# Optimization experiments

Hardware: AMD Instinct MI355X
Metric: run time of the kernel (lower is better)

## Reference

```python
import jax, jax.numpy as jnp
import numpy as np

N, E, IN, OUT = 50000, 800000, 256, 256
EPS = 1e-5


def setup_inputs() -> dict:
    key = jax.random.key(0)
    k1, k2, k3 = jax.random.split(key, 3)
    x = jax.random.normal(k1, (N, IN), dtype=jnp.float32)
    edge_index = jax.random.randint(k2, (2, E), 0, N, dtype=jnp.int64)
    batch = jnp.zeros((N,), dtype=jnp.int64)
    # glorot-style init for GCN weight
    scale = jnp.sqrt(2.0 / (IN + OUT)).astype(jnp.float32)
    W = jax.random.normal(k3, (IN, OUT), dtype=jnp.float32) * scale
    conv_bias = jnp.zeros((OUT,), dtype=jnp.float32)
    ln_weight = jnp.ones((OUT,), dtype=jnp.float32)
    ln_bias = jnp.zeros((OUT,), dtype=jnp.float32)
    prelu_a = jnp.full((1,), 0.25, dtype=jnp.float32)  # nn.PReLU default
    return {"x": x, "edge_index": edge_index, "batch": batch, "W": W,
            "conv_bias": conv_bias, "ln_weight": ln_weight,
            "ln_bias": ln_bias, "prelu_a": prelu_a}


def reference(x, edge_index, batch, W, conv_bias, ln_weight, ln_bias, prelu_a):
    n = x.shape[0]
    src, dst = edge_index[0], edge_index[1]
    # GCNConv: add self-loops, symmetric deg^{-1/2} normalization
    loop = jnp.arange(n, dtype=src.dtype)
    src_f = jnp.concatenate([src, loop])  # [E+N]
    dst_f = jnp.concatenate([dst, loop])
    h = x @ W  # [N, OUT] -- transform before propagate (PyG order)
    deg = jax.ops.segment_sum(jnp.ones_like(dst_f, dtype=h.dtype), dst_f,
                              num_segments=n)  # >=1 due to self loops
    dinv = jax.lax.rsqrt(deg)
    norm = dinv[src_f] * dinv[dst_f]  # [E+N]
    out = jax.ops.segment_sum(h[src_f] * norm[:, None], dst_f,
                              num_segments=n) + conv_bias  # [N, OUT]
    # PyG LayerNorm, mode='graph', batch=None: normalize over ALL nodes+feats
    mu = out.mean()
    xc = out - mu
    std = jnp.sqrt((xc * xc).mean())
    y = xc / (std + EPS) * ln_weight + ln_bias
    # PReLU (single shared slope)
    return jnp.where(y >= 0, y, prelu_a * y)
```

## Files before the change

### kernel.cpp

```cpp
#include <hip/hip_runtime.h>
#include <hip/hip_bf16.h>


#define F 256
#define EPSV 1e-5f

typedef __attribute__((ext_vector_type(8))) short short8;
typedef __attribute__((ext_vector_type(4))) float f32x4;

__device__ __forceinline__ unsigned short f2bf(float f) {
  union { float f; unsigned u; } v; v.f = f;
  unsigned r = v.u + 0x7fffu + ((v.u >> 16) & 1u);
  return (unsigned short)(r >> 16);
}

__device__ __forceinline__ float bf2f(unsigned short u) {
  union { unsigned u; float f; } v; v.u = ((unsigned)u) << 16; return v.f;
}


__global__ void init_prep(int* __restrict__ deg_cnt, int N, int NB,
                          const float* __restrict__ W, unsigned short* __restrict__ Wb) {
  if ((int)blockIdx.x < NB) {
    int i = blockIdx.x * 256 + threadIdx.x;
    if (i < N) deg_cnt[i] = 0;
    return;
  }
  int gid = (blockIdx.x - NB) * 256 + threadIdx.x;
  int j = gid & 7;
  int lane = (gid >> 3) & 63;
  int kc = (gid >> 9) & 7;
  int tt = gid >> 12;
  int k = kc * 32 + (lane >> 4) * 8 + j;
  int n = tt * 16 + (lane & 15);
  Wb[gid] = f2bf(W[k * 256 + n]);
}


__global__ void count_gemm(const int* __restrict__ dst, int* __restrict__ deg_cnt,
                           int* __restrict__ rank, int E, int eb,
                           const float* __restrict__ x, const unsigned short* __restrict__ Wb,
                           ushort4* __restrict__ hb, int N) {
  __shared__ unsigned short A[64][264];

  if ((int)blockIdx.x < eb) {
    int e = blockIdx.x * 256 + threadIdx.x;
    if (e < E) rank[e] = atomicAdd(&deg_cnt[dst[e]], 1);
    return;
  }

  int bid = blockIdx.x - eb;
  int m0 = bid * 64;
  int t = threadIdx.x;
  int lane = t & 63;
  int wave = t >> 6;
  int q = lane >> 4;

#pragma unroll
  for (int j = 0; j < 16; ++j) {
    int idx = j * 256 + t;
    int row = idx >> 6;
    int c4 = idx & 63;
    int gr = m0 + row;
    int grc = gr < N ? gr : N - 1;
    f32x4 v = __builtin_nontemporal_load((const f32x4*)(x + (size_t)grc * F + c4 * 4));
    ushort4 u;
    u.x = f2bf(v[0]); u.y = f2bf(v[1]); u.z = f2bf(v[2]); u.w = f2bf(v[3]);
    *(ushort4*)&A[row][c4 * 4] = u;
  }
  __syncthreads();

  f32x4 acc[4][4];
#pragma unroll
  for (int m = 0; m < 4; ++m)
#pragma unroll
    for (int tt = 0; tt < 4; ++tt)
      acc[m][tt] = (f32x4){0.f, 0.f, 0.f, 0.f};

  int arow = lane & 15;
  for (int kc = 0; kc < 8; ++kc) {
    short8 a[4];
#pragma unroll
    for (int m = 0; m < 4; ++m)
      a[m] = *(const short8*)&A[m * 16 + arow][kc * 32 + q * 8];
#pragma unroll
    for (int tt = 0; tt < 4; ++tt) {
      const short8 b = *(const short8*)(Wb + (((wave * 4 + tt) * 8 + kc) * 64 + lane) * 8);
#pragma unroll
      for (int m = 0; m < 4; ++m)
        acc[m][tt] = __builtin_amdgcn_mfma_f32_16x16x32_bf16(a[m], b, acc[m][tt], 0, 0, 0);
    }
  }

  __syncthreads();

  int ccol = lane & 15;
#pragma unroll
  for (int m = 0; m < 4; ++m) {
#pragma unroll
    for (int rr = 0; rr < 4; ++rr) {
      int lrow = m * 16 + q * 4 + rr;
#pragma unroll
      for (int tt = 0; tt < 4; ++tt)
        A[lrow][(wave * 4 + tt) * 16 + ccol] = f2bf(acc[m][tt][rr]);
    }
  }
  __syncthreads();
#pragma unroll
  for (int j = 0; j < 16; ++j) {
    int idx = j * 256 + t;
    int row = idx >> 6;
    int c4 = idx & 63;
    int grow = m0 + row;
    if (grow < N) hb[(size_t)grow * 64 + c4] = *(const ushort4*)&A[row][c4 * 4];
  }
}


__global__ void block_sums(const int* __restrict__ deg_cnt, int* __restrict__ bsum,
                           float* __restrict__ dinv, int N) {
  __shared__ int s[256];
  int t = threadIdx.x;
  int i = blockIdx.x * 256 + t;
  int d = (i < N) ? deg_cnt[i] : 0;
  if (i < N) dinv[i] = rsqrtf((float)(d + 1));
  s[t] = d;
  __syncthreads();
  for (int off = 128; off > 0; off >>= 1) {
    if (t < off) s[t] += s[t + off];
    __syncthreads();
  }
  if (t == 0) bsum[blockIdx.x] = s[0];
}

__global__ void scan_bsums(const int* __restrict__ bsum, int* __restrict__ boff, int nb) {
  __shared__ int s[256];
  int t = threadIdx.x;
  int v = (t < nb) ? bsum[t] : 0;
  s[t] = v;
  __syncthreads();
  for (int off = 1; off < 256; off <<= 1) {
    int x = (t >= off) ? s[t - off] : 0;
    __syncthreads();
    s[t] += x;
    __syncthreads();
  }
  if (t < nb) boff[t] = s[t] - v;
}

__global__ void write_csr(const int* __restrict__ deg_cnt, const int* __restrict__ boff,
                          int* __restrict__ csr_ptr, int N, int E) {
  __shared__ int s[256];
  int t = threadIdx.x;
  int i = blockIdx.x * 256 + t;
  int v = (i < N) ? deg_cnt[i] : 0;
  s[t] = v;
  __syncthreads();
  for (int off = 1; off < 256; off <<= 1) {
    int x = (t >= off) ? s[t - off] : 0;
    __syncthreads();
    s[t] += x;
    __syncthreads();
  }
  if (i < N) csr_ptr[i] = boff[blockIdx.x] + s[t] - v;
  if (i == 0) csr_ptr[N] = E;
}


__global__ void fill(const int* __restrict__ src, const int* __restrict__ dst,
                     const int* __restrict__ rank, const int* __restrict__ csr_ptr,
                     int* __restrict__ csr_src, int E) {
  int e = blockIdx.x * 256 + threadIdx.x;
  if (e < E) {
    int d = dst[e];
    csr_src[csr_ptr[d] + rank[e]] = src[e];
  }
}


__global__ void aggregate(const ushort4* __restrict__ hb, const int* __restrict__ csr_ptr,
                          const int* __restrict__ csr_src, const float* __restrict__ dinv,
                          const float* __restrict__ conv_bias, float* __restrict__ out,
                          double2* __restrict__ partials, int N) {
  int wave = threadIdx.x >> 6;
  int lane = threadIdx.x & 63;
  int row = blockIdx.x * 4 + wave;
  float s1 = 0.f, s2 = 0.f;

  if (row < N) {
    float di = dinv[row];
    int b0 = csr_ptr[row], b1 = csr_ptr[row + 1];
    ushort4 self = hb[(size_t)row * 64 + lane];
    f32x4 acc;
    acc[0] = bf2f(self.x) * di; acc[1] = bf2f(self.y) * di;
    acc[2] = bf2f(self.z) * di; acc[3] = bf2f(self.w) * di;

    for (int e = b0; e < b1; e += 16) {
      int idx[16];
#pragma unroll
      for (int j = 0; j < 16; ++j) {
        int ee = e + j;
        idx[j] = csr_src[ee < b1 ? ee : b1 - 1];
      }
      ushort4 v[16];
#pragma unroll
      for (int j = 0; j < 16; ++j) v[j] = hb[(size_t)idx[j] * 64 + lane];
      float w[16];
#pragma unroll
      for (int j = 0; j < 16; ++j) w[j] = dinv[idx[j]];
#pragma unroll
      for (int j = 0; j < 16; ++j) {
        float m = (e + j < b1) ? w[j] : 0.f;
        acc[0] = fmaf(bf2f(v[j].x), m, acc[0]);
        acc[1] = fmaf(bf2f(v[j].y), m, acc[1]);
        acc[2] = fmaf(bf2f(v[j].z), m, acc[2]);
        acc[3] = fmaf(bf2f(v[j].w), m, acc[3]);
      }
    }

    const f32x4 b = *(const f32x4*)(conv_bias + lane * 4);
    acc[0] = fmaf(acc[0], di, b[0]);
    acc[1] = fmaf(acc[1], di, b[1]);
    acc[2] = fmaf(acc[2], di, b[2]);
    acc[3] = fmaf(acc[3], di, b[3]);
    __builtin_nontemporal_store(acc, (f32x4*)(out + ((size_t)row * 64 + lane) * 4));
    s1 = acc[0] + acc[1] + acc[2] + acc[3];
    s2 = acc[0] * acc[0] + acc[1] * acc[1] + acc[2] * acc[2] + acc[3] * acc[3];
  }

  __shared__ float r1[256];
  __shared__ float r2[256];
  int t = threadIdx.x;
  r1[t] = s1;
  r2[t] = s2;
  __syncthreads();
  for (int off = 128; off > 0; off >>= 1) {
    if (t < off) { r1[t] += r1[t + off]; r2[t] += r2[t + off]; }
    __syncthreads();
  }
  if (t == 0) {
    double2 pp;
    pp.x = (double)r1[0];
    pp.y = (double)r2[0];
    partials[blockIdx.x] = pp;
  }
}

__global__ void finalize_stats(const double2* __restrict__ partials, int nb,
                               float* __restrict__ stats, double cnt) {
  __shared__ double q1[1024];
  __shared__ double q2[1024];
  int t = threadIdx.x;
  double a1 = 0.0, a2 = 0.0;
  for (int i = t; i < nb; i += 1024) {
    double2 pp = partials[i];
    a1 += pp.x;
    a2 += pp.y;
  }
  q1[t] = a1;
  q2[t] = a2;
  __syncthreads();
  for (int off = 512; off > 0; off >>= 1) {
    if (t < off) { q1[t] += q1[t + off]; q2[t] += q2[t + off]; }
    __syncthreads();
  }
  if (t == 0) {
    double mu = q1[0] / cnt;
    double var = q2[0] / cnt - mu * mu;
    if (var < 0) var = 0;
    double sd = sqrt(var);
    stats[0] = (float)mu;
    stats[1] = (float)(1.0 / (sd + (double)EPSV));
  }
}

__global__ void norm_prelu(float* __restrict__ out, const float* __restrict__ stats,
                           const float* __restrict__ lw, const float* __restrict__ lb,
                           const float* __restrict__ pa, int n4) {
  int i = blockIdx.x * blockDim.x + threadIdx.x;
  if (i >= n4) return;
  float mu = stats[0];
  float inv = stats[1];
  float a = pa[0];
  int c4 = (i & 63) * 4;
  const f32x4 w = *(const f32x4*)(lw + c4);
  const f32x4 b = *(const f32x4*)(lb + c4);
  f32x4 v = __builtin_nontemporal_load((const f32x4*)(out + (size_t)i * 4));
  f32x4 y;
#pragma unroll
  for (int j = 0; j < 4; ++j) {
    float yv = (v[j] - mu) * inv * w[j] + b[j];
    y[j] = yv >= 0.f ? yv : a * yv;
  }
  __builtin_nontemporal_store(y, (f32x4*)(out + (size_t)i * 4));
}


extern "C" void kernel_launch(void* const* d_in, const int* in_sizes, int n_in,
                              void* d_out, int out_size, void* d_ws, size_t ws_size,
                              hipStream_t stream) {
  const float* x = (const float*)d_in[0];
  const int* eidx = (const int*)d_in[1];
  const float* W = (const float*)d_in[3];
  const float* conv_bias = (const float*)d_in[4];
  const float* ln_w = (const float*)d_in[5];
  const float* ln_b = (const float*)d_in[6];
  const float* prelu_a = (const float*)d_in[7];
  float* out = (float*)d_out;

  int N = in_sizes[0] / F;
  int E = in_sizes[1] / 2;
  const int* src = eidx;
  const int* dst = eidx + E;

  int nAggBlocks = (N + 3) / 4;
  int eb = (E + 255) / 256;
  int gemmb = (N + 63) / 64;
  int NB = (N + 255) / 256;

  char* p = (char*)d_ws;
  auto carve = [&](size_t bytes) { char* r = p; p += (bytes + 255) & ~(size_t)255; return r; };
  ushort4* hb    = (ushort4*)carve((size_t)N * 64 * sizeof(ushort4));
  unsigned short* Wb = (unsigned short*)carve((size_t)F * F * sizeof(short));
  int* deg_cnt   = (int*)carve((size_t)N * sizeof(int));
  int* rank      = (int*)carve((size_t)E * sizeof(int));
  float* dinv    = (float*)carve((size_t)N * sizeof(float));
  int* csr_ptr   = (int*)carve((size_t)(N + 1) * sizeof(int));
  int* csr_src   = (int*)carve((size_t)E * sizeof(int));
  int* bsum      = (int*)carve((size_t)NB * sizeof(int));
  int* boff      = (int*)carve((size_t)NB * sizeof(int));
  double2* partials = (double2*)carve((size_t)nAggBlocks * sizeof(double2));
  float* stats   = (float*)carve(2 * sizeof(float));

  init_prep<<<NB + 256, 256, 0, stream>>>(deg_cnt, N, NB, W, Wb);
  count_gemm<<<eb + gemmb, 256, 0, stream>>>(dst, deg_cnt, rank, E, eb, x, Wb, hb, N);
  block_sums<<<NB, 256, 0, stream>>>(deg_cnt, bsum, dinv, N);
  scan_bsums<<<1, 256, 0, stream>>>(bsum, boff, NB);
  write_csr<<<NB, 256, 0, stream>>>(deg_cnt, boff, csr_ptr, N, E);
  fill<<<eb, 256, 0, stream>>>(src, dst, rank, csr_ptr, csr_src, E);
  aggregate<<<nAggBlocks, 256, 0, stream>>>(hb, csr_ptr, csr_src, dinv,
                                            conv_bias, out, partials, N);
  finalize_stats<<<1, 1024, 0, stream>>>(partials, nAggBlocks, stats,
                                         (double)N * (double)F);
  int n4 = N * (F / 4);
  norm_prelu<<<(n4 + 255) / 256, 256, 0, stream>>>(out, stats, ln_w, ln_b, prelu_a, n4);
}
```

Measured before the change: 276.7 us.

## Cut launches via atomic-based CSR build and atomic global stats

Replaces the three-kernel prefix scan with a single kernel that takes block offsets through an atomic base counter, so CSR segments are contiguous but not in node order. The per-edge rank array is dropped and fill now claims slots with atomics on csr_ptr; aggregate recovers each row's range from the end pointer and the degree. The finalize_stats kernel is removed: aggregate blocks atomically add double partial sums, and every norm_prelu thread recomputes mean and inverse std. This removes two to three launches and the rank traffic, at the cost of atomic contention, nondeterministic neighbour order, and per-thread double math.

```diff
diff --git a/kernel.cpp b/kernel.cpp
--- a/kernel.cpp
+++ b/kernel.cpp
@@ -20,10 +20,16 @@
 
 
 __global__ void init_prep(int* __restrict__ deg_cnt, int N, int NB,
-                          const float* __restrict__ W, unsigned short* __restrict__ Wb) {
+                          const float* __restrict__ W, unsigned short* __restrict__ Wb,
+                          int* __restrict__ gbase, double* __restrict__ gsum) {
   if ((int)blockIdx.x < NB) {
     int i = blockIdx.x * 256 + threadIdx.x;
     if (i < N) deg_cnt[i] = 0;
+    if (blockIdx.x == 0 && threadIdx.x == 0) {
+      *gbase = 0;
+      gsum[0] = 0.0;
+      gsum[1] = 0.0;
+    }
     return;
   }
   int gid = (blockIdx.x - NB) * 256 + threadIdx.x;
@@ -38,14 +44,14 @@
 
 
 __global__ void count_gemm(const int* __restrict__ dst, int* __restrict__ deg_cnt,
-                           int* __restrict__ rank, int E, int eb,
+                           int E, int eb,
                            const float* __restrict__ x, const unsigned short* __restrict__ Wb,
                            ushort4* __restrict__ hb, int N) {
   __shared__ unsigned short A[64][264];
 
   if ((int)blockIdx.x < eb) {
     int e = blockIdx.x * 256 + threadIdx.x;
-    if (e < E) rank[e] = atomicAdd(&deg_cnt[dst[e]], 1);
+    if (e < E) atomicAdd(&deg_cnt[dst[e]], 1);
     return;
   }
 
@@ -117,71 +123,42 @@
 }
 
 
-__global__ void block_sums(const int* __restrict__ deg_cnt, int* __restrict__ bsum,
-                           float* __restrict__ dinv, int N) {
+__global__ void build_ptr(const int* __restrict__ deg_cnt, float* __restrict__ dinv,
+                          int* __restrict__ csr_ptr, int* __restrict__ gbase, int N) {
   __shared__ int s[256];
+  __shared__ int base;
   int t = threadIdx.x;
   int i = blockIdx.x * 256 + t;
   int d = (i < N) ? deg_cnt[i] : 0;
   if (i < N) dinv[i] = rsqrtf((float)(d + 1));
   s[t] = d;
   __syncthreads();
-  for (int off = 128; off > 0; off >>= 1) {
-    if (t < off) s[t] += s[t + off];
-    __syncthreads();
-  }
-  if (t == 0) bsum[blockIdx.x] = s[0];
-}
-
-__global__ void scan_bsums(const int* __restrict__ bsum, int* __restrict__ boff, int nb) {
-  __shared__ int s[256];
-  int t = threadIdx.x;
-  int v = (t < nb) ? bsum[t] : 0;
-  s[t] = v;
-  __syncthreads();
   for (int off = 1; off < 256; off <<= 1) {
     int x = (t >= off) ? s[t - off] : 0;
     __syncthreads();
     s[t] += x;
     __syncthreads();
   }
-  if (t < nb) boff[t] = s[t] - v;
-}
-
-__global__ void write_csr(const int* __restrict__ deg_cnt, const int* __restrict__ boff,
-                          int* __restrict__ csr_ptr, int N, int E) {
-  __shared__ int s[256];
-  int t = threadIdx.x;
-  int i = blockIdx.x * 256 + t;
-  int v = (i < N) ? deg_cnt[i] : 0;
-  s[t] = v;
-  __syncthreads();
-  for (int off = 1; off < 256; off <<= 1) {
-    int x = (t >= off) ? s[t - off] : 0;
-    __syncthreads();
-    s[t] += x;
-    __syncthreads();
-  }
-  if (i < N) csr_ptr[i] = boff[blockIdx.x] + s[t] - v;
-  if (i == 0) csr_ptr[N] = E;
+  if (t == 255) base = atomicAdd(gbase, s[255]);
+  __syncthreads();
+  if (i < N) csr_ptr[i] = base + s[t] - d;
 }
 
 
 __global__ void fill(const int* __restrict__ src, const int* __restrict__ dst,
-                     const int* __restrict__ rank, const int* __restrict__ csr_ptr,
-                     int* __restrict__ csr_src, int E) {
+                     int* __restrict__ csr_ptr, int* __restrict__ csr_src, int E) {
   int e = blockIdx.x * 256 + threadIdx.x;
   if (e < E) {
-    int d = dst[e];
-    csr_src[csr_ptr[d] + rank[e]] = src[e];
+    int pos = atomicAdd(&csr_ptr[dst[e]], 1);
+    csr_src[pos] = src[e];
   }
 }
 
 
 __global__ void aggregate(const ushort4* __restrict__ hb, const int* __restrict__ csr_ptr,
-                          const int* __restrict__ csr_src, const float* __restrict__ dinv,
-                          const float* __restrict__ conv_bias, float* __restrict__ out,
-                          double2* __restrict__ partials, int N) {
+                          const int* __restrict__ deg_cnt, const int* __restrict__ csr_src,
+                          const float* __restrict__ dinv, const float* __restrict__ conv_bias,
+                          float* __restrict__ out, double* __restrict__ gsum, int N) {
   int wave = threadIdx.x >> 6;
   int lane = threadIdx.x & 63;
   int row = blockIdx.x * 4 + wave;
@@ -189,7 +166,8 @@
 
   if (row < N) {
     float di = dinv[row];
-    int b0 = csr_ptr[row], b1 = csr_ptr[row + 1];
+    int b1 = csr_ptr[row];
+    int b0 = b1 - deg_cnt[row];
     ushort4 self = hb[(size_t)row * 64 + lane];
     f32x4 acc;
     acc[0] = bf2f(self.x) * di; acc[1] = bf2f(self.y) * di;
@@ -239,48 +217,24 @@
     __syncthreads();
   }
   if (t == 0) {
-    double2 pp;
-    pp.x = (double)r1[0];
-    pp.y = (double)r2[0];
-    partials[blockIdx.x] = pp;
-  }
-}
-
-__global__ void finalize_stats(const double2* __restrict__ partials, int nb,
-                               float* __restrict__ stats, double cnt) {
-  __shared__ double q1[1024];
-  __shared__ double q2[1024];
-  int t = threadIdx.x;
-  double a1 = 0.0, a2 = 0.0;
-  for (int i = t; i < nb; i += 1024) {
-    double2 pp = partials[i];
-    a1 += pp.x;
-    a2 += pp.y;
-  }
-  q1[t] = a1;
-  q2[t] = a2;
-  __syncthreads();
-  for (int off = 512; off > 0; off >>= 1) {
-    if (t < off) { q1[t] += q1[t + off]; q2[t] += q2[t + off]; }
-    __syncthreads();
-  }
-  if (t == 0) {
-    double mu = q1[0] / cnt;
-    double var = q2[0] / cnt - mu * mu;
-    if (var < 0) var = 0;
-    double sd = sqrt(var);
-    stats[0] = (float)mu;
-    stats[1] = (float)(1.0 / (sd + (double)EPSV));
-  }
-}
-
-__global__ void norm_prelu(float* __restrict__ out, const float* __restrict__ stats,
+    atomicAdd(&gsum[0], (double)r1[0]);
+    atomicAdd(&gsum[1], (double)r2[0]);
+  }
+}
+
+
+__global__ void norm_prelu(float* __restrict__ out, const double* __restrict__ gsum,
                            const float* __restrict__ lw, const float* __restrict__ lb,
-                           const float* __restrict__ pa, int n4) {
+                           const float* __restrict__ pa, int n4, double cnt) {
   int i = blockIdx.x * blockDim.x + threadIdx.x;
   if (i >= n4) return;
-  float mu = stats[0];
-  float inv = stats[1];
+  double g1 = gsum[0];
+  double g2 = gsum[1];
+  double mud = g1 / cnt;
+  double var = g2 / cnt - mud * mud;
+  if (var < 0) var = 0;
+  float mu = (float)mud;
+  float inv = (float)(1.0 / (sqrt(var) + (double)EPSV));
   float a = pa[0];
   int c4 = (i & 63) * 4;
   const f32x4 w = *(const f32x4*)(lw + c4);
@@ -323,25 +277,19 @@
   ushort4* hb    = (ushort4*)carve((size_t)N * 64 * sizeof(ushort4));
   unsigned short* Wb = (unsigned short*)carve((size_t)F * F * sizeof(short));
   int* deg_cnt   = (int*)carve((size_t)N * sizeof(int));
-  int* rank      = (int*)carve((size_t)E * sizeof(int));
   float* dinv    = (float*)carve((size_t)N * sizeof(float));
-  int* csr_ptr   = (int*)carve((size_t)(N + 1) * sizeof(int));
+  int* csr_ptr   = (int*)carve((size_t)N * sizeof(int));
   int* csr_src   = (int*)carve((size_t)E * sizeof(int));
-  int* bsum      = (int*)carve((size_t)NB * sizeof(int));
-  int* boff      = (int*)carve((size_t)NB * sizeof(int));
-  double2* partials = (double2*)carve((size_t)nAggBlocks * sizeof(double2));
-  float* stats   = (float*)carve(2 * sizeof(float));
-
-  init_prep<<<NB + 256, 256, 0, stream>>>(deg_cnt, N, NB, W, Wb);
-  count_gemm<<<eb + gemmb, 256, 0, stream>>>(dst, deg_cnt, rank, E, eb, x, Wb, hb, N);
-  block_sums<<<NB, 256, 0, stream>>>(deg_cnt, bsum, dinv, N);
-  scan_bsums<<<1, 256, 0, stream>>>(bsum, boff, NB);
-  write_csr<<<NB, 256, 0, stream>>>(deg_cnt, boff, csr_ptr, N, E);
-  fill<<<eb, 256, 0, stream>>>(src, dst, rank, csr_ptr, csr_src, E);
-  aggregate<<<nAggBlocks, 256, 0, stream>>>(hb, csr_ptr, csr_src, dinv,
-                                            conv_bias, out, partials, N);
-  finalize_stats<<<1, 1024, 0, stream>>>(partials, nAggBlocks, stats,
-                                         (double)N * (double)F);
+  int* gbase     = (int*)carve(sizeof(int));
+  double* gsum   = (double*)carve(2 * sizeof(double));
+
+  init_prep<<<NB + 256, 256, 0, stream>>>(deg_cnt, N, NB, W, Wb, gbase, gsum);
+  count_gemm<<<eb + gemmb, 256, 0, stream>>>(dst, deg_cnt, E, eb, x, Wb, hb, N);
+  build_ptr<<<NB, 256, 0, stream>>>(deg_cnt, dinv, csr_ptr, gbase, N);
+  fill<<<eb, 256, 0, stream>>>(src, dst, csr_ptr, csr_src, E);
+  aggregate<<<nAggBlocks, 256, 0, stream>>>(hb, csr_ptr, deg_cnt, csr_src, dinv,
+                                            conv_bias, out, gsum, N);
   int n4 = N * (F / 4);
-  norm_prelu<<<(n4 + 255) / 256, 256, 0, stream>>>(out, stats, ln_w, ln_b, prelu_a, n4);
-}
+  norm_prelu<<<(n4 + 255) / 256, 256, 0, stream>>>(out, gsum, ln_w, ln_b, prelu_a,
+                                                   n4, (double)N * (double)F);
+}
```

New measurement: 534.1 us. 93.0% more time.

## Split aggregate waves into half-wave rows and fuse stats finalize into norm kernel

Applied to the files above, without the earlier changes.

The aggregate kernel now gives each half-wave one destination row, with each lane loading 16-byte bf16 chunks. A wave therefore handles two rows and fetches wider gathers, and the neighbor loop is unrolled by 8 instead of 16. The separate finalize_stats kernel is removed: each of 256 blocks of the norm_prelu kernel reduces the partial sums itself, then applies normalization and PReLU in a grid-stride loop. This saves one launch and the stats round trip, at the cost of redundant per-block reduction work over the partials.

```diff
diff --git a/kernel.cpp b/kernel.cpp
--- a/kernel.cpp
+++ b/kernel.cpp
@@ -6,6 +6,7 @@
 #define EPSV 1e-5f
 
 typedef __attribute__((ext_vector_type(8))) short short8;
+typedef __attribute__((ext_vector_type(8))) unsigned short ushort8v;
 typedef __attribute__((ext_vector_type(4))) float f32x4;
 
 __device__ __forceinline__ unsigned short f2bf(float f) {
@@ -49,8 +50,7 @@
     return;
   }
 
-  int bid = blockIdx.x - eb;
-  int m0 = bid * 64;
+  int m0 = (blockIdx.x - eb) * 64;
   int t = threadIdx.x;
   int lane = t & 63;
   int wave = t >> 6;
@@ -91,7 +91,6 @@
         acc[m][tt] = __builtin_amdgcn_mfma_f32_16x16x32_bf16(a[m], b, acc[m][tt], 0, 0, 0);
     }
   }
-
   __syncthreads();
 
   int ccol = lane & 15;
@@ -184,48 +183,59 @@
                           double2* __restrict__ partials, int N) {
   int wave = threadIdx.x >> 6;
   int lane = threadIdx.x & 63;
-  int row = blockIdx.x * 4 + wave;
+  int half = lane >> 5;
+  int l = lane & 31;
+  int row = blockIdx.x * 8 + wave * 2 + half;
   float s1 = 0.f, s2 = 0.f;
+  const unsigned short* hbs = (const unsigned short*)hb;
 
   if (row < N) {
     float di = dinv[row];
     int b0 = csr_ptr[row], b1 = csr_ptr[row + 1];
-    ushort4 self = hb[(size_t)row * 64 + lane];
-    f32x4 acc;
-    acc[0] = bf2f(self.x) * di; acc[1] = bf2f(self.y) * di;
-    acc[2] = bf2f(self.z) * di; acc[3] = bf2f(self.w) * di;
-
-    for (int e = b0; e < b1; e += 16) {
-      int idx[16];
-#pragma unroll
-      for (int j = 0; j < 16; ++j) {
+    ushort8v sv = *(const ushort8v*)(hbs + (size_t)row * 256 + l * 8);
+    float acc[8];
+#pragma unroll
+    for (int c = 0; c < 8; ++c) acc[c] = bf2f(sv[c]) * di;
+
+    for (int e = b0; e < b1; e += 8) {
+      int idx[8];
+#pragma unroll
+      for (int j = 0; j < 8; ++j) {
         int ee = e + j;
         idx[j] = csr_src[ee < b1 ? ee : b1 - 1];
       }
-      ushort4 v[16];
-#pragma unroll
-      for (int j = 0; j < 16; ++j) v[j] = hb[(size_t)idx[j] * 64 + lane];
-      float w[16];
-#pragma unroll
-      for (int j = 0; j < 16; ++j) w[j] = dinv[idx[j]];
-#pragma unroll
-      for (int j = 0; j < 16; ++j) {
+      ushort8v v[8];
+#pragma unroll
+      for (int j = 0; j < 8; ++j)
+        v[j] = *(const ushort8v*)(hbs + (size_t)idx[j] * 256 + l * 8);
+      float w[8];
+#pragma unroll
+      for (int j = 0; j < 8; ++j) w[j] = dinv[idx[j]];
+#pragma unroll
+      for (int j = 0; j < 8; ++j) {
         float m = (e + j < b1) ? w[j] : 0.f;
-        acc[0] = fmaf(bf2f(v[j].x), m, acc[0]);
-        acc[1] = fmaf(bf2f(v[j].y), m, acc[1]);
-        acc[2] = fmaf(bf2f(v[j].z), m, acc[2]);
-        acc[3] = fmaf(bf2f(v[j].w), m, acc[3]);
+#pragma unroll
+        for (int c = 0; c < 8; ++c)
+          acc[c] = fmaf(bf2f(v[j][c]), m, acc[c]);
       }
     }
 
-    const f32x4 b = *(const f32x4*)(conv_bias + lane * 4);
-    acc[0] = fmaf(acc[0], di, b[0]);
-    acc[1] = fmaf(acc[1], di, b[1]);
-    acc[2] = fmaf(acc[2], di, b[2]);
-    acc[3] = fmaf(acc[3], di, b[3]);
-    __builtin_nontemporal_store(acc, (f32x4*)(out + ((size_t)row * 64 + lane) * 4));
-    s1 = acc[0] + acc[1] + acc[2] + acc[3];
-    s2 = acc[0] * acc[0] + acc[1] * acc[1] + acc[2] * acc[2] + acc[3] * acc[3];
+    const f32x4 ba = *(const f32x4*)(conv_bias + l * 8);
+    const f32x4 bb = *(const f32x4*)(conv_bias + l * 8 + 4);
+    f32x4 o0, o1;
+#pragma unroll
+    for (int c = 0; c < 4; ++c) {
+      o0[c] = fmaf(acc[c], di, ba[c]);
+      o1[c] = fmaf(acc[c + 4], di, bb[c]);
+    }
+    float* orow = out + (size_t)row * 256 + l * 8;
+    __builtin_nontemporal_store(o0, (f32x4*)orow);
+    __builtin_nontemporal_store(o1, (f32x4*)(orow + 4));
+#pragma unroll
+    for (int c = 0; c < 4; ++c) {
+      s1 += o0[c] + o1[c];
+      s2 += o0[c] * o0[c] + o1[c] * o1[c];
+    }
   }
 
   __shared__ float r1[256];
@@ -246,10 +256,13 @@
   }
 }
 
-__global__ void finalize_stats(const double2* __restrict__ partials, int nb,
-                               float* __restrict__ stats, double cnt) {
+
+__global__ void norm_prelu(float* __restrict__ out, const double2* __restrict__ partials,
+                           int nb, const float* __restrict__ lw, const float* __restrict__ lb,
+                           const float* __restrict__ pa, int n4, double cnt) {
   __shared__ double q1[1024];
   __shared__ double q2[1024];
+  __shared__ float sstats[2];
   int t = threadIdx.x;
   double a1 = 0.0, a2 = 0.0;
   for (int i = t; i < nb; i += 1024) {
@@ -268,31 +281,27 @@
     double mu = q1[0] / cnt;
     double var = q2[0] / cnt - mu * mu;
     if (var < 0) var = 0;
-    double sd = sqrt(var);
-    stats[0] = (float)mu;
-    stats[1] = (float)(1.0 / (sd + (double)EPSV));
-  }
-}
-
-__global__ void norm_prelu(float* __restrict__ out, const float* __restrict__ stats,
-                           const float* __restrict__ lw, const float* __restrict__ lb,
-                           const float* __restrict__ pa, int n4) {
-  int i = blockIdx.x * blockDim.x + threadIdx.x;
-  if (i >= n4) return;
-  float mu = stats[0];
-  float inv = stats[1];
+    sstats[0] = (float)mu;
+    sstats[1] = (float)(1.0 / (sqrt(var) + (double)EPSV));
+  }
+  __syncthreads();
+  float mu = sstats[0];
+  float inv = sstats[1];
   float a = pa[0];
-  int c4 = (i & 63) * 4;
-  const f32x4 w = *(const f32x4*)(lw + c4);
-  const f32x4 b = *(const f32x4*)(lb + c4);
-  f32x4 v = __builtin_nontemporal_load((const f32x4*)(out + (size_t)i * 4));
-  f32x4 y;
-#pragma unroll
-  for (int j = 0; j < 4; ++j) {
-    float yv = (v[j] - mu) * inv * w[j] + b[j];
-    y[j] = yv >= 0.f ? yv : a * yv;
-  }
-  __builtin_nontemporal_store(y, (f32x4*)(out + (size_t)i * 4));
+  int stride = gridDim.x * 1024;
+  for (int i = blockIdx.x * 1024 + t; i < n4; i += stride) {
+    int c4 = (i & 63) * 4;
+    const f32x4 w = *(const f32x4*)(lw + c4);
+    const f32x4 b = *(const f32x4*)(lb + c4);
+    f32x4 v = __builtin_nontemporal_load((const f32x4*)(out + (size_t)i * 4));
+    f32x4 y;
+#pragma unroll
+    for (int j = 0; j < 4; ++j) {
+      float yv = (v[j] - mu) * inv * w[j] + b[j];
+      y[j] = yv >= 0.f ? yv : a * yv;
+    }
+    __builtin_nontemporal_store(y, (f32x4*)(out + (size_t)i * 4));
+  }
 }
 
 
@@ -313,7 +322,7 @@
   const int* src = eidx;
   const int* dst = eidx + E;
 
-  int nAggBlocks = (N + 3) / 4;
+  int nAggBlocks = (N + 7) / 8;
   int eb = (E + 255) / 256;
   int gemmb = (N + 63) / 64;
   int NB = (N + 255) / 256;
@@ -330,7 +339,6 @@
   int* bsum      = (int*)carve((size_t)NB * sizeof(int));
   int* boff      = (int*)carve((size_t)NB * sizeof(int));
   double2* partials = (double2*)carve((size_t)nAggBlocks * sizeof(double2));
-  float* stats   = (float*)carve(2 * sizeof(float));
 
   init_prep<<<NB + 256, 256, 0, stream>>>(deg_cnt, N, NB, W, Wb);
   count_gemm<<<eb + gemmb, 256, 0, stream>>>(dst, deg_cnt, rank, E, eb, x, Wb, hb, N);
@@ -340,8 +348,7 @@
   fill<<<eb, 256, 0, stream>>>(src, dst, rank, csr_ptr, csr_src, E);
   aggregate<<<nAggBlocks, 256, 0, stream>>>(hb, csr_ptr, csr_src, dinv,
                                             conv_bias, out, partials, N);
-  finalize_stats<<<1, 1024, 0, stream>>>(partials, nAggBlocks, stats,
-                                         (double)N * (double)F);
   int n4 = N * (F / 4);
-  norm_prelu<<<(n4 + 255) / 256, 256, 0, stream>>>(out, stats, ln_w, ln_b, prelu_a, n4);
-}
+  norm_prelu<<<256, 1024, 0, stream>>>(out, partials, nAggBlocks, ln_w, ln_b, prelu_a,
+                                       n4, (double)N * (double)F);
+}
```

Result: faster. 268.2 us (-3.1%).
